# Kernel optimization log

Hardware: AMD Instinct MI355X
Metric: run time of the kernel (lower is better)

The kernel has to match this reference:

```python
import jax, jax.numpy as jnp
from jax import lax
import numpy as np

FEAT_STRIDE = 16
PRE_NMS_TOP_N = 2000
POST_NMS_TOP_N = 300
NMS_THRESH = 0.7


def _whctrs(a):
    w = a[2] - a[0] + 1.0
    h = a[3] - a[1] + 1.0
    return w, h, a[0] + 0.5 * (w - 1.0), a[1] + 0.5 * (h - 1.0)


def _mkanchors(ws, hs, x_ctr, y_ctr):
    ws = np.asarray(ws, dtype=np.float64)
    hs = np.asarray(hs, dtype=np.float64)
    return np.stack([x_ctr - 0.5 * (ws - 1.0), y_ctr - 0.5 * (hs - 1.0),
                     x_ctr + 0.5 * (ws - 1.0), y_ctr + 0.5 * (hs - 1.0)], axis=1)


def generate_anchors(base_size=16, ratios=np.array([0.5, 1.0, 2.0]), scales=np.array([8.0, 16.0, 32.0])):
    base = np.array([1.0, 1.0, float(base_size), float(base_size)]) - 1.0
    w, h, xc, yc = _whctrs(base)
    size = w * h
    ws = np.round(np.sqrt(size / ratios))
    hs = np.round(ws * ratios)
    ratio_anchors = _mkanchors(ws, hs, xc, yc)
    out = []
    for i in range(ratio_anchors.shape[0]):
        w_i, h_i, xc_i, yc_i = _whctrs(ratio_anchors[i])
        out.append(_mkanchors(w_i * scales, h_i * scales, xc_i, yc_i))
    return np.vstack(out).astype(np.float32)


ANCHORS = generate_anchors()  # [A=9, 4]
NUM_ANCHORS = ANCHORS.shape[0]


def _nms_keep(boxes, thresh):
    # boxes [N,4], already sorted by descending score; torchvision IoU convention.
    x1, y1, x2, y2 = boxes[:, 0], boxes[:, 1], boxes[:, 2], boxes[:, 3]
    areas = (x2 - x1) * (y2 - y1)
    xx1 = jnp.maximum(x1[:, None], x1[None, :])
    yy1 = jnp.maximum(y1[:, None], y1[None, :])
    xx2 = jnp.minimum(x2[:, None], x2[None, :])
    yy2 = jnp.minimum(y2[:, None], y2[None, :])
    inter = jnp.clip(xx2 - xx1, 0.0) * jnp.clip(yy2 - yy1, 0.0)
    iou = inter / (areas[:, None] + areas[None, :] - inter + 1e-9)
    n = boxes.shape[0]
    # sup[i, j] True => box i (higher score) suppresses later box j
    sup = (iou > thresh) & jnp.triu(jnp.ones((n, n), bool), 1)

    def body(i, keep):
        return keep & ~(keep[i] & sup[i])

    return lax.fori_loop(0, n, body, jnp.ones((n,), bool))


def setup_inputs() -> dict:
    key = jax.random.key(0)
    k1, k2 = jax.random.split(key)
    B, A, H, W = 8, NUM_ANCHORS, 128, 128
    scores = jax.random.normal(k1, (B, 2 * A, H, W), jnp.float32)
    bbox_deltas = jax.random.normal(k2, (B, 4 * A, H, W), jnp.float32) * 0.2
    im_h = float(H * FEAT_STRIDE)
    im_w = float(W * FEAT_STRIDE)
    im_info = jnp.tile(jnp.array([[im_h, im_w, 1.0]], jnp.float32), (B, 1))
    return {"scores": scores, "bbox_deltas": bbox_deltas, "im_info": im_info}


def reference(scores, bbox_deltas, im_info):
    B, _, H, W = scores.shape
    A = NUM_ANCHORS
    # --- anchor generation over the feature grid ---
    sx = jnp.arange(W, dtype=jnp.float32) * FEAT_STRIDE
    sy = jnp.arange(H, dtype=jnp.float32) * FEAT_STRIDE
    gx, gy = jnp.meshgrid(sx, sy)  # 'xy' indexing matches np.meshgrid default
    shifts = jnp.stack([gx.ravel(), gy.ravel(), gx.ravel(), gy.ravel()], axis=1)  # [K,4]
    anchors = (jnp.asarray(ANCHORS)[None, :, :] + shifts[:, None, :]).reshape(-1, 4)  # [K*A,4]

    obj_scores = scores[:, A:].transpose(0, 2, 3, 1).reshape(B, -1)   # [B, K*A]
    deltas = bbox_deltas.transpose(0, 2, 3, 1).reshape(B, -1, 4)      # [B, K*A, 4]

    # --- bbox_transform_inv ---
    widths = anchors[:, 2] - anchors[:, 0] + 1.0
    heights = anchors[:, 3] - anchors[:, 1] + 1.0
    ctr_x = anchors[:, 0] + 0.5 * widths
    ctr_y = anchors[:, 1] + 0.5 * heights
    dx, dy, dw, dh = deltas[..., 0], deltas[..., 1], deltas[..., 2], deltas[..., 3]
    pred_ctr_x = dx * widths + ctr_x
    pred_ctr_y = dy * heights + ctr_y
    pred_w = jnp.exp(dw) * widths
    pred_h = jnp.exp(dh) * heights
    proposals = jnp.stack([pred_ctr_x - 0.5 * pred_w, pred_ctr_y - 0.5 * pred_h,
                           pred_ctr_x + 0.5 * pred_w, pred_ctr_y + 0.5 * pred_h], axis=-1)

    # --- clip_boxes: im_info[b] = (h, w, scale) ---
    max_x = (im_info[:, 1] - 1.0)[:, None]
    max_y = (im_info[:, 0] - 1.0)[:, None]
    proposals = jnp.stack([
        jnp.clip(proposals[..., 0], 0.0, max_x),
        jnp.clip(proposals[..., 1], 0.0, max_y),
        jnp.clip(proposals[..., 2], 0.0, max_x),
        jnp.clip(proposals[..., 3], 0.0, max_y)], axis=-1)

    # --- pre-NMS top-k by score ---
    _, order = lax.top_k(obj_scores, PRE_NMS_TOP_N)                  # [B, pre]
    top_props = jnp.take_along_axis(proposals, order[..., None], axis=1)  # [B, pre, 4]

    # --- per-image greedy NMS (fixed-size, jit-compatible) ---
    keep = jax.vmap(lambda b: _nms_keep(b, NMS_THRESH))(top_props)   # [B, pre] bool
    sel = jnp.argsort(jnp.where(keep, 0, 1), axis=1, stable=True)[:, :POST_NMS_TOP_N]
    valid = jnp.take_along_axis(keep, sel, axis=1)                   # [B, post]
    out_boxes = jnp.take_along_axis(top_props, sel[..., None], axis=1) * valid[..., None].astype(top_props.dtype)

    batch_idx = jnp.broadcast_to(
        jnp.arange(B, dtype=out_boxes.dtype)[:, None, None], (B, POST_NMS_TOP_N, 1))
    return jnp.concatenate([batch_idx, out_boxes], axis=-1)  # [B, post_nms_topN, 5]
```

## Files before the change

kernel.cpp:

```cpp
#include <hip/hip_runtime.h>

#define NB 8
#define NA 9
#define NCELL (128 * 128)
#define NTOT (NCELL * NA)
#define PRE_K 2000
#define POST_K 300
#define PARTS 18
#define SLOT 512
#define THR_BIN 0x5FFu
#define NMS_TH 0.7f

__constant__ float c_aw[NA] = {184.f, 368.f, 736.f, 128.f, 256.f, 512.f, 88.f, 176.f, 352.f};
__constant__ float c_ah[NA] = {96.f, 192.f, 384.f, 128.f, 256.f, 512.f, 176.f, 352.f, 704.f};

__device__ __forceinline__ unsigned int sortable(float s) {
    unsigned int u = __float_as_uint(s);
    return (u & 0x80000000u) ? ~u : (u | 0x80000000u);
}

__device__ __forceinline__ unsigned long long shflx64(unsigned long long v, int m) {
    return __shfl_xor(v, m, 64);
}

__device__ __forceinline__ float4 decode_box(unsigned int i, const float* __restrict__ dbase,
                                             float maxx, float maxy) {
    unsigned int cell = i / 9u;
    unsigned int a = i - cell * 9u;
    int wx = (int)(cell & 127u), hy = (int)(cell >> 7);
    const float* dp = dbase + (size_t)(4u * a) * NCELL + (size_t)hy * 128 + wx;
    float dx = dp[0];
    float dy = dp[NCELL];
    float dw = dp[2 * NCELL];
    float dh = dp[3 * NCELL];
    float W_ = c_aw[a], H_ = c_ah[a];
    float cx = (float)(16 * wx + 8), cy = (float)(16 * hy + 8);
    float px = __fadd_rn(__fmul_rn(dx, W_), cx);
    float py = __fadd_rn(__fmul_rn(dy, H_), cy);
    float pw = __fmul_rn((float)exp((double)dw), W_);
    float ph = __fmul_rn((float)exp((double)dh), H_);
    float hw = __fmul_rn(0.5f, pw), hh = __fmul_rn(0.5f, ph);
    float x1 = __fsub_rn(px, hw), y1 = __fsub_rn(py, hh);
    float x2 = __fadd_rn(px, hw), y2 = __fadd_rn(py, hh);
    x1 = fminf(fmaxf(x1, 0.0f), maxx);
    y1 = fminf(fmaxf(y1, 0.0f), maxy);
    x2 = fminf(fmaxf(x2, 0.0f), maxx);
    y2 = fminf(fmaxf(y2, 0.0f), maxy);
    return make_float4(x1, y1, x2, y2);
}

__global__ __launch_bounds__(1024) void sweep_kernel(const float* __restrict__ scores,
                                                     unsigned int* __restrict__ h0out,
                                                     int* __restrict__ bcnt,
                                                     unsigned long long* __restrict__ buf) {
    __shared__ unsigned int h[2048];
    __shared__ unsigned long long lbuf[SLOT];
    __shared__ int lcnt;
    int b = blockIdx.y, part = blockIdx.x, tid = threadIdx.x;
    h[tid] = 0; h[tid + 1024] = 0;
    if (tid == 0) lcnt = 0;
    __syncthreads();
    const float4* sp4 = (const float4*)(scores + (size_t)b * 18 * NCELL + (size_t)NA * NCELL);
    int base4 = part * 2048;
#pragma unroll
    for (int e = 0; e < 2; ++e) {
        int t4 = base4 + e * 1024 + tid;
        float4 v = sp4[t4];
        float el[4] = {v.x, v.y, v.z, v.w};
#pragma unroll
        for (int j = 0; j < 4; ++j) {
            unsigned int u = sortable(el[j]);
            atomicAdd(&h[u >> 21], 1u);
            if ((u >> 21) >= THR_BIN) {
                int idx4 = t4 * 4 + j;
                int a = idx4 >> 14;
                int cell = idx4 & 16383;
                unsigned int i = (unsigned int)cell * 9u + (unsigned int)a;
                int pos = atomicAdd(&lcnt, 1);
                if (pos < SLOT)
                    lbuf[pos] = ((unsigned long long)u << 32) |
                                (unsigned long long)(0xFFFFFFFFu - i);
            }
        }
    }
    __syncthreads();
    unsigned int* o = h0out + ((size_t)(b * PARTS + part)) * 2048;
    o[tid] = h[tid];
    o[tid + 1024] = h[tid + 1024];
    if (tid == 0) bcnt[b * PARTS + part] = lcnt;
    int m = min(lcnt, SLOT);
    for (int t = tid; t < m; t += 1024)
        buf[((size_t)(b * PARTS + part)) * SLOT + t] = lbuf[t];
}

#define SHFL_STEP(J)                                                          \
    {                                                                         \
        int d_ = (J) >> 1;                                                    \
        bool keepMax = (((tid & d_) == 0) == (((2u * (unsigned)tid) & k) == 0)); \
        unsigned long long pa = shflx64(va, d_);                              \
        unsigned long long pb = shflx64(vb, d_);                              \
        va = keepMax ? (va > pa ? va : pa) : (va < pa ? va : pa);             \
        vb = keepMax ? (vb > pb ? vb : pb) : (vb < pb ? vb : pb);             \
    }
#define LOCAL_STEP()                                                          \
    {                                                                         \
        bool desc = (((2u * (unsigned)tid) & k) == 0);                        \
        unsigned long long lo = va < vb ? va : vb;                            \
        unsigned long long hi = va < vb ? vb : va;                            \
        va = desc ? hi : lo; vb = desc ? lo : hi;                             \
    }

__global__ __launch_bounds__(1024) void sortdec_kernel(const float* __restrict__ scores,
                                                       const unsigned int* __restrict__ h0out,
                                                       const int* __restrict__ bcnt,
                                                       const unsigned long long* __restrict__ buf,
                                                       unsigned int* __restrict__ topidx) {
    __shared__ unsigned long long s[4096];
    __shared__ unsigned int wpart[16], wexcl[16];
    __shared__ unsigned int h128[128];
    __shared__ int sbc[PARTS];
    __shared__ unsigned int sh_piv, sh_spiv;
    __shared__ unsigned int sh_need;
    __shared__ int sh_ok, fcnt;
    int b = blockIdx.x, tid = threadIdx.x;
    int lane = tid & 63, wid = tid >> 6;
    unsigned int* thr = (unsigned int*)s;

    if (tid < PARTS) sbc[tid] = bcnt[b * PARTS + tid];
    if (tid == 0) { sh_ok = 1; fcnt = 0; }

    unsigned int c0 = 0, c1 = 0;
#pragma unroll
    for (int p = 0; p < PARTS; ++p) {
        const unsigned int* hp = h0out + ((size_t)(b * PARTS + p)) * 2048;
        uint2 v = *(const uint2*)&hp[2 * tid];
        c0 += v.x; c1 += v.y;
    }
    unsigned int sum = c0 + c1;
#pragma unroll
    for (int off = 1; off < 64; off <<= 1) {
        unsigned int v = __shfl_down(sum, off, 64);
        if (lane + off < 64) sum += v;
    }
    if (lane == 0) wpart[wid] = sum;
    __syncthreads();
    if (tid < 16) {
        unsigned int e = 0;
        for (int w = tid + 1; w < 16; ++w) e += wpart[w];
        wexcl[tid] = e;
    }
    __syncthreads();
    unsigned int self = sum + wexcl[wid];
    thr[tid] = self;
    __syncthreads();
    unsigned int above = (tid < 1023) ? thr[tid + 1] : 0u;
    if (self >= (unsigned)PRE_K && above < (unsigned)PRE_K) {
        if (above + c1 >= (unsigned)PRE_K) {
            sh_piv = (unsigned)(2 * tid + 1); sh_need = (unsigned)(PRE_K)-above;
        } else {
            sh_piv = (unsigned)(2 * tid); sh_need = (unsigned)(PRE_K)-above - c1;
        }
    }
    __syncthreads();
    unsigned int piv = sh_piv;
    if (tid < PARTS && sbc[tid] > SLOT) sh_ok = 0;
    if (tid == 0 && piv < THR_BIN) sh_ok = 0;
    if (tid < 128) h128[tid] = 0;
    __syncthreads();
    int ok = sh_ok;

    if (ok) {
        for (int t = tid; t < PARTS * SLOT; t += 1024) {
            int p = t >> 9, off = t & (SLOT - 1);
            if (off < sbc[p]) {
                unsigned long long e = buf[((size_t)(b * PARTS + p)) * SLOT + off];
                unsigned int u = (unsigned int)(e >> 32);
                if ((u >> 21) == piv) atomicAdd(&h128[(u >> 14) & 127u], 1u);
            }
        }
    } else {
        const float4* sp4 = (const float4*)(scores + (size_t)b * 18 * NCELL + (size_t)NA * NCELL);
        for (int t = tid; t < NTOT / 4; t += 1024) {
            float4 v = sp4[t];
            unsigned int u;
            u = sortable(v.x); if ((u >> 21) == piv) atomicAdd(&h128[(u >> 14) & 127u], 1u);
            u = sortable(v.y); if ((u >> 21) == piv) atomicAdd(&h128[(u >> 14) & 127u], 1u);
            u = sortable(v.z); if ((u >> 21) == piv) atomicAdd(&h128[(u >> 14) & 127u], 1u);
            u = sortable(v.w); if ((u >> 21) == piv) atomicAdd(&h128[(u >> 14) & 127u], 1u);
        }
    }
    __syncthreads();
    if (tid < 64) {
        unsigned int d0 = h128[2 * lane], d1 = h128[2 * lane + 1];
        unsigned int rs = d0 + d1;
#pragma unroll
        for (int off = 1; off < 64; off <<= 1) {
            unsigned int v = __shfl_down(rs, off, 64);
            if (lane + off < 64) rs += v;
        }
        unsigned int rab = __shfl_down(rs, 1, 64);
        if (lane == 63) rab = 0;
        unsigned int need0 = sh_need;
        if (rs >= need0 && rab < need0) {
            unsigned int d = (rab + d1 >= need0) ? (unsigned)(2 * lane + 1) : (unsigned)(2 * lane);
            sh_spiv = ((piv << 7) | d) << 14;
        }
    }
    __syncthreads();
    unsigned int spiv = sh_spiv;

    if (ok) {
        for (int t = tid; t < PARTS * SLOT; t += 1024) {
            int p = t >> 9, off = t & (SLOT - 1);
            if (off < sbc[p]) {
                unsigned long long e = buf[((size_t)(b * PARTS + p)) * SLOT + off];
                if ((unsigned int)(e >> 32) >= spiv) {
                    int pos = atomicAdd(&fcnt, 1);
                    if (pos < 4096) s[pos] = e;
                }
            }
        }
    } else {
        const float4* sp4 = (const float4*)(scores + (size_t)b * 18 * NCELL + (size_t)NA * NCELL);
        for (int t4 = tid; t4 < NTOT / 4; t4 += 1024) {
            float4 v = sp4[t4];
            float el[4] = {v.x, v.y, v.z, v.w};
#pragma unroll
            for (int j = 0; j < 4; ++j) {
                unsigned int u = sortable(el[j]);
                if (u >= spiv) {
                    int idx4 = t4 * 4 + j;
                    int a = idx4 >> 14;
                    int cell = idx4 & 16383;
                    unsigned int i = (unsigned int)cell * 9u + (unsigned int)a;
                    int pos = atomicAdd(&fcnt, 1);
                    if (pos < 4096)
                        s[pos] = ((unsigned long long)u << 32) |
                                 (unsigned long long)(0xFFFFFFFFu - i);
                }
            }
        }
    }
    __syncthreads();
    int n2 = min(fcnt, 4096);
    int SZ = (n2 <= 2048) ? 2048 : 4096;
    for (int t = tid; t < SZ; t += 1024)
        if (t >= n2) s[t] = 0ULL;
    __syncthreads();

    if (SZ == 2048) {
        unsigned long long va = s[2 * tid], vb = s[2 * tid + 1];
#pragma unroll
        for (unsigned k = 2; k <= 128; k <<= 1) {
#pragma unroll
            for (unsigned j = k >> 1; j >= 2; j >>= 1) SHFL_STEP(j)
            LOCAL_STEP()
        }
        for (unsigned k = 256; k <= 2048; k <<= 1) {
            s[2 * tid] = va; s[2 * tid + 1] = vb;
            __syncthreads();
            for (unsigned j = k >> 1; j >= 128; j >>= 1) {
                for (int t = tid; t < 2048; t += 1024) {
                    int ixj = t ^ (int)j;
                    if (ixj > t) {
                        unsigned long long x = s[t], y = s[ixj];
                        if ((((unsigned)t & k) == 0) ? (x < y) : (x > y)) { s[t] = y; s[ixj] = x; }
                    }
                }
                __syncthreads();
            }
            va = s[2 * tid]; vb = s[2 * tid + 1];
#pragma unroll
            for (unsigned j = 64; j >= 2; j >>= 1) SHFL_STEP(j)
            LOCAL_STEP()
        }
        s[2 * tid] = va; s[2 * tid + 1] = vb;
        __syncthreads();
    } else {
        for (int k = 2; k <= 4096; k <<= 1) {
            for (int j = k >> 1; j > 0; j >>= 1) {
                for (int t = tid; t < 4096; t += 1024) {
                    int ixj = t ^ j;
                    if (ixj > t) {
                        unsigned long long x = s[t], y = s[ixj];
                        if (((t & k) == 0) ? (x < y) : (x > y)) { s[t] = y; s[ixj] = x; }
                    }
                }
                __syncthreads();
            }
        }
    }
    for (int r = tid; r < PRE_K; r += 1024)
        topidx[(size_t)b * PRE_K + r] = 0xFFFFFFFFu - (unsigned int)(s[r] & 0xFFFFFFFFu);
}

__global__ void mask_kernel(const unsigned int* __restrict__ topidx,
                            const float* __restrict__ deltas,
                            const float* __restrict__ im_info,
                            unsigned long long* __restrict__ colm) {
    int iT = blockIdx.x, jT = blockIdx.y, b = blockIdx.z;
    if (iT > jT) return;
    __shared__ float4 ib[64];
    int t = threadIdx.x;
    float maxx = __fsub_rn(im_info[b * 3 + 1], 1.0f);
    float maxy = __fsub_rn(im_info[b * 3 + 0], 1.0f);
    const float* dbase = deltas + (size_t)b * 36 * NCELL;
    const unsigned int* ti = topidx + (size_t)b * PRE_K;
    int i0 = iT * 64;
    ib[t] = (i0 + t < PRE_K) ? decode_box(ti[i0 + t], dbase, maxx, maxy)
                             : make_float4(0.f, 0.f, -1.f, -1.f);
    int j = jT * 64 + t;
    bool jv = j < PRE_K;
    float4 jb = jv ? decode_box(ti[j], dbase, maxx, maxy) : make_float4(0.f, 0.f, -1.f, -1.f);
    __syncthreads();
    if (!jv) return;
    float barea = __fmul_rn(__fsub_rn(jb.z, jb.x), __fsub_rn(jb.w, jb.y));
    unsigned long long m = 0ULL;
    for (int ii = 0; ii < 64; ++ii) {
        int i = i0 + ii;
        if (i < j) {
            float4 c = ib[ii];
            float aarea = __fmul_rn(__fsub_rn(c.z, c.x), __fsub_rn(c.w, c.y));
            float xx1 = fmaxf(c.x, jb.x), yy1 = fmaxf(c.y, jb.y);
            float xx2 = fminf(c.z, jb.z), yy2 = fminf(c.w, jb.w);
            float iw = fmaxf(__fsub_rn(xx2, xx1), 0.0f);
            float ih = fmaxf(__fsub_rn(yy2, yy1), 0.0f);
            float inter = __fmul_rn(iw, ih);
            float denom = __fadd_rn(__fsub_rn(__fadd_rn(aarea, barea), inter), 1e-9f);
            float iou = __fdiv_rn(inter, denom);
            if (iou > NMS_TH) m |= (1ULL << ii);
        }
    }
    colm[((size_t)b * 32 + iT) * 2048 + j] = m;
}

#define PROCESS_TILE(K, BUF)                                                   \
    {                                                                          \
        unsigned long long diag = 0ULL;                                        \
        _Pragma("unroll") for (int q = 0; q < 32; ++q)                         \
            if (q == (K)) diag = BUF[q];                                       \
        int j = (K) * 64 + lane;                                               \
        bool alive_me = (((dead >> (K)) & 1u) == 0u) && (j < PRE_K);           \
        unsigned long long alive = __ballot(alive_me);                         \
        unsigned long long keptw = 0ULL;                                       \
        while (alive) {                                                        \
            int i = __builtin_ctzll(alive);                                    \
            keptw |= (1ULL << i);                                              \
            if (lane == 0 && total < POST_K) keeplist[total] = (K) * 64 + i;   \
            total++;                                                           \
            if (total >= POST_K) { done = true; break; }                       \
            unsigned long long sup = __ballot(((diag >> i) & 1ULL) != 0ULL);   \
            alive &= ~sup;                                                     \
            alive &= ~keptw;                                                   \
        }                                                                      \
        _Pragma("unroll") for (int q = 0; q < 32; ++q)                         \
            if (q > (K) && ((BUF[q] & keptw) != 0ULL)) dead |= (1u << q);      \
    }

__global__ __launch_bounds__(64) void scan_kernel(const unsigned long long* __restrict__ colm,
                                                  const unsigned int* __restrict__ topidx,
                                                  const float* __restrict__ deltas,
                                                  const float* __restrict__ im_info,
                                                  float* __restrict__ out) {
    __shared__ int keeplist[POST_K];
    int b = blockIdx.x, lane = threadIdx.x;
    const unsigned long long* cb = colm + (size_t)b * 32 * 2048;
    unsigned int dead = 0;
    int total = 0;
    bool done = false;
    unsigned long long bufA[32], bufB[32];
#pragma unroll
    for (int q = 0; q < 32; ++q) bufA[q] = cb[q * 64 + lane];
    for (int kk = 0; kk < 16 && !done; ++kk) {
        int k0 = 2 * kk;
#pragma unroll
        for (int q = 0; q < 32; ++q)
            bufB[q] = cb[(size_t)(k0 + 1) * 2048 + q * 64 + lane];
        PROCESS_TILE(k0, bufA)
        if (done) break;
        int k1 = k0 + 1;
        if (k1 + 1 < 32) {
#pragma unroll
            for (int q = 0; q < 32; ++q)
                bufA[q] = cb[(size_t)(k1 + 1) * 2048 + q * 64 + lane];
        }
        PROCESS_TILE(k1, bufB)
    }
    __syncthreads();
    int K = min(total, POST_K);
    float maxx = __fsub_rn(im_info[b * 3 + 1], 1.0f);
    float maxy = __fsub_rn(im_info[b * 3 + 0], 1.0f);
    const float* dbase = deltas + (size_t)b * 36 * NCELL;
    const unsigned int* ti = topidx + (size_t)b * PRE_K;
    for (int r = lane; r < POST_K; r += 64) {
        float4 v = make_float4(0.f, 0.f, 0.f, 0.f);
        if (r < K) v = decode_box(ti[keeplist[r]], dbase, maxx, maxy);
        float* o = out + ((size_t)b * POST_K + r) * 5;
        o[0] = (float)b;
        o[1] = v.x;
        o[2] = v.y;
        o[3] = v.z;
        o[4] = v.w;
    }
}

extern "C" void kernel_launch(void* const* d_in, const int* in_sizes, int n_in,
                              void* d_out, int out_size, void* d_ws, size_t ws_size,
                              hipStream_t stream) {
    const float* scores = (const float*)d_in[0];
    const float* deltas = (const float*)d_in[1];
    const float* im_info = (const float*)d_in[2];
    float* out = (float*)d_out;
    char* ws = (char*)d_ws;

    unsigned int* h0out = (unsigned int*)(ws + 0);
    int* bcnt = (int*)(ws + 1179648);
    unsigned long long* buf = (unsigned long long*)(ws + 1180672);
    unsigned int* topidx = (unsigned int*)(ws + 1770496);
    unsigned long long* colm = (unsigned long long*)(ws + 1834496);

    hipLaunchKernelGGL(sweep_kernel, dim3(PARTS, NB), dim3(1024), 0, stream,
                       scores, h0out, bcnt, buf);
    hipLaunchKernelGGL(sortdec_kernel, dim3(NB), dim3(1024), 0, stream,
                       scores, h0out, bcnt, buf, topidx);
    hipLaunchKernelGGL(mask_kernel, dim3(32, 32, NB), dim3(64), 0, stream,
                       topidx, deltas, im_info, colm);
    hipLaunchKernelGGL(scan_kernel, dim3(NB), dim3(64), 0, stream,
                       colm, topidx, deltas, im_info, out);
}
```

Measured before the change: 106.9 us.

## Drop full-histogram output from sweep and precompute decoded boxes in separate kernel

The sweep kernel no longer builds or writes a 2048-bin histogram per partition. The sort kernel instead builds its coarse histogram from only the candidate buffer, falling back to a full rescan when the buffer overflows or holds fewer than PRE_K entries. A new decode kernel decodes the 2000 top boxes per image once into a float4 array, which the mask and scan kernels then read instead of recomputing exp-based decoding per tile. This adds one kernel launch and removes redundant double-precision exp work and histogram atomics and traffic.

```diff
diff --git a/kernel.cpp b/kernel.cpp
--- a/kernel.cpp
+++ b/kernel.cpp
@@ -23,12 +23,276 @@
     return __shfl_xor(v, m, 64);
 }
 
-__device__ __forceinline__ float4 decode_box(unsigned int i, const float* __restrict__ dbase,
-                                             float maxx, float maxy) {
+__global__ __launch_bounds__(1024) void sweep_kernel(const float* __restrict__ scores,
+                                                     int* __restrict__ bcnt,
+                                                     unsigned long long* __restrict__ buf) {
+    __shared__ unsigned long long lbuf[SLOT];
+    __shared__ int lcnt;
+    int b = blockIdx.y, part = blockIdx.x, tid = threadIdx.x;
+    if (tid == 0) lcnt = 0;
+    __syncthreads();
+    const float4* sp4 = (const float4*)(scores + (size_t)b * 18 * NCELL + (size_t)NA * NCELL);
+    int base4 = part * 2048;
+#pragma unroll
+    for (int e = 0; e < 2; ++e) {
+        int t4 = base4 + e * 1024 + tid;
+        float4 v = sp4[t4];
+        float el[4] = {v.x, v.y, v.z, v.w};
+#pragma unroll
+        for (int j = 0; j < 4; ++j) {
+            unsigned int u = sortable(el[j]);
+            if ((u >> 21) >= THR_BIN) {
+                int idx4 = t4 * 4 + j;
+                int a = idx4 >> 14;
+                int cell = idx4 & 16383;
+                unsigned int i = (unsigned int)cell * 9u + (unsigned int)a;
+                int pos = atomicAdd(&lcnt, 1);
+                if (pos < SLOT)
+                    lbuf[pos] = ((unsigned long long)u << 32) |
+                                (unsigned long long)(0xFFFFFFFFu - i);
+            }
+        }
+    }
+    __syncthreads();
+    if (tid == 0) bcnt[b * PARTS + part] = lcnt;
+    int m = min(lcnt, SLOT);
+    for (int t = tid; t < m; t += 1024)
+        buf[((size_t)(b * PARTS + part)) * SLOT + t] = lbuf[t];
+}
+
+#define SHFL_STEP(J)                                                          \
+    {                                                                         \
+        int d_ = (J) >> 1;                                                    \
+        bool keepMax = (((tid & d_) == 0) == (((2u * (unsigned)tid) & k) == 0)); \
+        unsigned long long pa = shflx64(va, d_);                              \
+        unsigned long long pb = shflx64(vb, d_);                              \
+        va = keepMax ? (va > pa ? va : pa) : (va < pa ? va : pa);             \
+        vb = keepMax ? (vb > pb ? vb : pb) : (vb < pb ? vb : pb);             \
+    }
+#define LOCAL_STEP()                                                          \
+    {                                                                         \
+        bool desc = (((2u * (unsigned)tid) & k) == 0);                        \
+        unsigned long long lo = va < vb ? va : vb;                            \
+        unsigned long long hi = va < vb ? vb : va;                            \
+        va = desc ? hi : lo; vb = desc ? lo : hi;                             \
+    }
+
+__global__ __launch_bounds__(1024) void sortdec_kernel(const float* __restrict__ scores,
+                                                       const int* __restrict__ bcnt,
+                                                       const unsigned long long* __restrict__ buf,
+                                                       unsigned int* __restrict__ topidx) {
+    __shared__ unsigned long long s[4096];
+    __shared__ unsigned int wpart[16], wexcl[16];
+    __shared__ unsigned int h128[128];
+    __shared__ int sbc[PARTS];
+    __shared__ unsigned int sh_piv, sh_spiv;
+    __shared__ unsigned int sh_need;
+    __shared__ int sh_ok, fcnt;
+    int b = blockIdx.x, tid = threadIdx.x;
+    int lane = tid & 63, wid = tid >> 6;
+    unsigned int* hist2 = (unsigned int*)s;
+    unsigned int* thr = ((unsigned int*)s) + 2048;
+
+    if (tid < PARTS) sbc[tid] = bcnt[b * PARTS + tid];
+    if (tid == 0) fcnt = 0;
+    hist2[tid] = 0; hist2[tid + 1024] = 0;
+    __syncthreads();
+    if (tid == 0) {
+        int okv = 1, tot = 0;
+        for (int p = 0; p < PARTS; ++p) { if (sbc[p] > SLOT) okv = 0; tot += sbc[p]; }
+        if (tot < PRE_K) okv = 0;
+        sh_ok = okv;
+    }
+    __syncthreads();
+    int ok = sh_ok;
+
+    if (ok) {
+        for (int t = tid; t < PARTS * SLOT; t += 1024) {
+            int p = t >> 9, off = t & (SLOT - 1);
+            if (off < sbc[p]) {
+                unsigned int u = (unsigned int)(buf[((size_t)(b * PARTS + p)) * SLOT + off] >> 32);
+                atomicAdd(&hist2[u >> 21], 1u);
+            }
+        }
+    } else {
+        const float4* sp4 = (const float4*)(scores + (size_t)b * 18 * NCELL + (size_t)NA * NCELL);
+        for (int t = tid; t < NTOT / 4; t += 1024) {
+            float4 v = sp4[t];
+            atomicAdd(&hist2[sortable(v.x) >> 21], 1u);
+            atomicAdd(&hist2[sortable(v.y) >> 21], 1u);
+            atomicAdd(&hist2[sortable(v.z) >> 21], 1u);
+            atomicAdd(&hist2[sortable(v.w) >> 21], 1u);
+        }
+    }
+    __syncthreads();
+    unsigned int c0 = hist2[2 * tid], c1 = hist2[2 * tid + 1];
+    unsigned int sum = c0 + c1;
+#pragma unroll
+    for (int off = 1; off < 64; off <<= 1) {
+        unsigned int v = __shfl_down(sum, off, 64);
+        if (lane + off < 64) sum += v;
+    }
+    if (lane == 0) wpart[wid] = sum;
+    __syncthreads();
+    if (tid < 16) {
+        unsigned int e = 0;
+        for (int w = tid + 1; w < 16; ++w) e += wpart[w];
+        wexcl[tid] = e;
+    }
+    __syncthreads();
+    unsigned int self = sum + wexcl[wid];
+    thr[tid] = self;
+    __syncthreads();
+    unsigned int above = (tid < 1023) ? thr[tid + 1] : 0u;
+    if (self >= (unsigned)PRE_K && above < (unsigned)PRE_K) {
+        if (above + c1 >= (unsigned)PRE_K) {
+            sh_piv = (unsigned)(2 * tid + 1); sh_need = (unsigned)(PRE_K)-above;
+        } else {
+            sh_piv = (unsigned)(2 * tid); sh_need = (unsigned)(PRE_K)-above - c1;
+        }
+    }
+    if (tid < 128) h128[tid] = 0;
+    __syncthreads();
+    unsigned int piv = sh_piv;
+
+    if (ok) {
+        for (int t = tid; t < PARTS * SLOT; t += 1024) {
+            int p = t >> 9, off = t & (SLOT - 1);
+            if (off < sbc[p]) {
+                unsigned long long e = buf[((size_t)(b * PARTS + p)) * SLOT + off];
+                unsigned int u = (unsigned int)(e >> 32);
+                if ((u >> 21) == piv) atomicAdd(&h128[(u >> 14) & 127u], 1u);
+            }
+        }
+    } else {
+        const float4* sp4 = (const float4*)(scores + (size_t)b * 18 * NCELL + (size_t)NA * NCELL);
+        for (int t = tid; t < NTOT / 4; t += 1024) {
+            float4 v = sp4[t];
+            unsigned int u;
+            u = sortable(v.x); if ((u >> 21) == piv) atomicAdd(&h128[(u >> 14) & 127u], 1u);
+            u = sortable(v.y); if ((u >> 21) == piv) atomicAdd(&h128[(u >> 14) & 127u], 1u);
+            u = sortable(v.z); if ((u >> 21) == piv) atomicAdd(&h128[(u >> 14) & 127u], 1u);
+            u = sortable(v.w); if ((u >> 21) == piv) atomicAdd(&h128[(u >> 14) & 127u], 1u);
+        }
+    }
+    __syncthreads();
+    if (tid < 64) {
+        unsigned int d0 = h128[2 * lane], d1 = h128[2 * lane + 1];
+        unsigned int rs = d0 + d1;
+#pragma unroll
+        for (int off = 1; off < 64; off <<= 1) {
+            unsigned int v = __shfl_down(rs, off, 64);
+            if (lane + off < 64) rs += v;
+        }
+        unsigned int rab = __shfl_down(rs, 1, 64);
+        if (lane == 63) rab = 0;
+        unsigned int need0 = sh_need;
+        if (rs >= need0 && rab < need0) {
+            unsigned int d = (rab + d1 >= need0) ? (unsigned)(2 * lane + 1) : (unsigned)(2 * lane);
+            sh_spiv = ((piv << 7) | d) << 14;
+        }
+    }
+    __syncthreads();
+    unsigned int spiv = sh_spiv;
+
+    if (ok) {
+        for (int t = tid; t < PARTS * SLOT; t += 1024) {
+            int p = t >> 9, off = t & (SLOT - 1);
+            if (off < sbc[p]) {
+                unsigned long long e = buf[((size_t)(b * PARTS + p)) * SLOT + off];
+                if ((unsigned int)(e >> 32) >= spiv) {
+                    int pos = atomicAdd(&fcnt, 1);
+                    if (pos < 4096) s[pos] = e;
+                }
+            }
+        }
+    } else {
+        const float4* sp4 = (const float4*)(scores + (size_t)b * 18 * NCELL + (size_t)NA * NCELL);
+        for (int t4 = tid; t4 < NTOT / 4; t4 += 1024) {
+            float4 v = sp4[t4];
+            float el[4] = {v.x, v.y, v.z, v.w};
+#pragma unroll
+            for (int j = 0; j < 4; ++j) {
+                unsigned int u = sortable(el[j]);
+                if (u >= spiv) {
+                    int idx4 = t4 * 4 + j;
+                    int a = idx4 >> 14;
+                    int cell = idx4 & 16383;
+                    unsigned int i = (unsigned int)cell * 9u + (unsigned int)a;
+                    int pos = atomicAdd(&fcnt, 1);
+                    if (pos < 4096)
+                        s[pos] = ((unsigned long long)u << 32) |
+                                 (unsigned long long)(0xFFFFFFFFu - i);
+                }
+            }
+        }
+    }
+    __syncthreads();
+    int n2 = min(fcnt, 4096);
+    int SZ = (n2 <= 2048) ? 2048 : 4096;
+    for (int t = tid; t < SZ; t += 1024)
+        if (t >= n2) s[t] = 0ULL;
+    __syncthreads();
+
+    if (SZ == 2048) {
+        unsigned long long va = s[2 * tid], vb = s[2 * tid + 1];
+#pragma unroll
+        for (unsigned k = 2; k <= 128; k <<= 1) {
+#pragma unroll
+            for (unsigned j = k >> 1; j >= 2; j >>= 1) SHFL_STEP(j)
+            LOCAL_STEP()
+        }
+        for (unsigned k = 256; k <= 2048; k <<= 1) {
+            s[2 * tid] = va; s[2 * tid + 1] = vb;
+            __syncthreads();
+            for (unsigned j = k >> 1; j >= 128; j >>= 1) {
+                for (int t = tid; t < 2048; t += 1024) {
+                    int ixj = t ^ (int)j;
+                    if (ixj > t) {
+                        unsigned long long x = s[t], y = s[ixj];
+                        if ((((unsigned)t & k) == 0) ? (x < y) : (x > y)) { s[t] = y; s[ixj] = x; }
+                    }
+                }
+                __syncthreads();
+            }
+            va = s[2 * tid]; vb = s[2 * tid + 1];
+#pragma unroll
+            for (unsigned j = 64; j >= 2; j >>= 1) SHFL_STEP(j)
+            LOCAL_STEP()
+        }
+        s[2 * tid] = va; s[2 * tid + 1] = vb;
+        __syncthreads();
+    } else {
+        for (int k = 2; k <= 4096; k <<= 1) {
+            for (int j = k >> 1; j > 0; j >>= 1) {
+                for (int t = tid; t < 4096; t += 1024) {
+                    int ixj = t ^ j;
+                    if (ixj > t) {
+                        unsigned long long x = s[t], y = s[ixj];
+                        if (((t & k) == 0) ? (x < y) : (x > y)) { s[t] = y; s[ixj] = x; }
+                    }
+                }
+                __syncthreads();
+            }
+        }
+    }
+    for (int r = tid; r < PRE_K; r += 1024)
+        topidx[(size_t)b * PRE_K + r] = 0xFFFFFFFFu - (unsigned int)(s[r] & 0xFFFFFFFFu);
+}
+
+__global__ void decode_kernel(const unsigned int* __restrict__ topidx,
+                              const float* __restrict__ deltas,
+                              const float* __restrict__ im_info,
+                              float4* __restrict__ props) {
+    int gid = blockIdx.x * 256 + threadIdx.x;
+    if (gid >= NB * PRE_K) return;
+    int b = gid / PRE_K;
+    unsigned int i = topidx[gid];
     unsigned int cell = i / 9u;
     unsigned int a = i - cell * 9u;
     int wx = (int)(cell & 127u), hy = (int)(cell >> 7);
-    const float* dp = dbase + (size_t)(4u * a) * NCELL + (size_t)hy * 128 + wx;
+    const float* dp = deltas + (size_t)b * 36 * NCELL + (size_t)(4u * a) * NCELL +
+                      (size_t)hy * 128 + wx;
     float dx = dp[0];
     float dy = dp[NCELL];
     float dw = dp[2 * NCELL];
@@ -42,278 +306,27 @@
     float hw = __fmul_rn(0.5f, pw), hh = __fmul_rn(0.5f, ph);
     float x1 = __fsub_rn(px, hw), y1 = __fsub_rn(py, hh);
     float x2 = __fadd_rn(px, hw), y2 = __fadd_rn(py, hh);
+    float maxx = __fsub_rn(im_info[b * 3 + 1], 1.0f);
+    float maxy = __fsub_rn(im_info[b * 3 + 0], 1.0f);
     x1 = fminf(fmaxf(x1, 0.0f), maxx);
     y1 = fminf(fmaxf(y1, 0.0f), maxy);
     x2 = fminf(fmaxf(x2, 0.0f), maxx);
     y2 = fminf(fmaxf(y2, 0.0f), maxy);
-    return make_float4(x1, y1, x2, y2);
-}
-
-__global__ __launch_bounds__(1024) void sweep_kernel(const float* __restrict__ scores,
-                                                     unsigned int* __restrict__ h0out,
-                                                     int* __restrict__ bcnt,
-                                                     unsigned long long* __restrict__ buf) {
-    __shared__ unsigned int h[2048];
-    __shared__ unsigned long long lbuf[SLOT];
-    __shared__ int lcnt;
-    int b = blockIdx.y, part = blockIdx.x, tid = threadIdx.x;
-    h[tid] = 0; h[tid + 1024] = 0;
-    if (tid == 0) lcnt = 0;
-    __syncthreads();
-    const float4* sp4 = (const float4*)(scores + (size_t)b * 18 * NCELL + (size_t)NA * NCELL);
-    int base4 = part * 2048;
-#pragma unroll
-    for (int e = 0; e < 2; ++e) {
-        int t4 = base4 + e * 1024 + tid;
-        float4 v = sp4[t4];
-        float el[4] = {v.x, v.y, v.z, v.w};
-#pragma unroll
-        for (int j = 0; j < 4; ++j) {
-            unsigned int u = sortable(el[j]);
-            atomicAdd(&h[u >> 21], 1u);
-            if ((u >> 21) >= THR_BIN) {
-                int idx4 = t4 * 4 + j;
-                int a = idx4 >> 14;
-                int cell = idx4 & 16383;
-                unsigned int i = (unsigned int)cell * 9u + (unsigned int)a;
-                int pos = atomicAdd(&lcnt, 1);
-                if (pos < SLOT)
-                    lbuf[pos] = ((unsigned long long)u << 32) |
-                                (unsigned long long)(0xFFFFFFFFu - i);
-            }
-        }
-    }
-    __syncthreads();
-    unsigned int* o = h0out + ((size_t)(b * PARTS + part)) * 2048;
-    o[tid] = h[tid];
-    o[tid + 1024] = h[tid + 1024];
-    if (tid == 0) bcnt[b * PARTS + part] = lcnt;
-    int m = min(lcnt, SLOT);
-    for (int t = tid; t < m; t += 1024)
-        buf[((size_t)(b * PARTS + part)) * SLOT + t] = lbuf[t];
-}
-
-#define SHFL_STEP(J)                                                          \
-    {                                                                         \
-        int d_ = (J) >> 1;                                                    \
-        bool keepMax = (((tid & d_) == 0) == (((2u * (unsigned)tid) & k) == 0)); \
-        unsigned long long pa = shflx64(va, d_);                              \
-        unsigned long long pb = shflx64(vb, d_);                              \
-        va = keepMax ? (va > pa ? va : pa) : (va < pa ? va : pa);             \
-        vb = keepMax ? (vb > pb ? vb : pb) : (vb < pb ? vb : pb);             \
-    }
-#define LOCAL_STEP()                                                          \
-    {                                                                         \
-        bool desc = (((2u * (unsigned)tid) & k) == 0);                        \
-        unsigned long long lo = va < vb ? va : vb;                            \
-        unsigned long long hi = va < vb ? vb : va;                            \
-        va = desc ? hi : lo; vb = desc ? lo : hi;                             \
-    }
-
-__global__ __launch_bounds__(1024) void sortdec_kernel(const float* __restrict__ scores,
-                                                       const unsigned int* __restrict__ h0out,
-                                                       const int* __restrict__ bcnt,
-                                                       const unsigned long long* __restrict__ buf,
-                                                       unsigned int* __restrict__ topidx) {
-    __shared__ unsigned long long s[4096];
-    __shared__ unsigned int wpart[16], wexcl[16];
-    __shared__ unsigned int h128[128];
-    __shared__ int sbc[PARTS];
-    __shared__ unsigned int sh_piv, sh_spiv;
-    __shared__ unsigned int sh_need;
-    __shared__ int sh_ok, fcnt;
-    int b = blockIdx.x, tid = threadIdx.x;
-    int lane = tid & 63, wid = tid >> 6;
-    unsigned int* thr = (unsigned int*)s;
-
-    if (tid < PARTS) sbc[tid] = bcnt[b * PARTS + tid];
-    if (tid == 0) { sh_ok = 1; fcnt = 0; }
-
-    unsigned int c0 = 0, c1 = 0;
-#pragma unroll
-    for (int p = 0; p < PARTS; ++p) {
-        const unsigned int* hp = h0out + ((size_t)(b * PARTS + p)) * 2048;
-        uint2 v = *(const uint2*)&hp[2 * tid];
-        c0 += v.x; c1 += v.y;
-    }
-    unsigned int sum = c0 + c1;
-#pragma unroll
-    for (int off = 1; off < 64; off <<= 1) {
-        unsigned int v = __shfl_down(sum, off, 64);
-        if (lane + off < 64) sum += v;
-    }
-    if (lane == 0) wpart[wid] = sum;
-    __syncthreads();
-    if (tid < 16) {
-        unsigned int e = 0;
-        for (int w = tid + 1; w < 16; ++w) e += wpart[w];
-        wexcl[tid] = e;
-    }
-    __syncthreads();
-    unsigned int self = sum + wexcl[wid];
-    thr[tid] = self;
-    __syncthreads();
-    unsigned int above = (tid < 1023) ? thr[tid + 1] : 0u;
-    if (self >= (unsigned)PRE_K && above < (unsigned)PRE_K) {
-        if (above + c1 >= (unsigned)PRE_K) {
-            sh_piv = (unsigned)(2 * tid + 1); sh_need = (unsigned)(PRE_K)-above;
-        } else {
-            sh_piv = (unsigned)(2 * tid); sh_need = (unsigned)(PRE_K)-above - c1;
-        }
-    }
-    __syncthreads();
-    unsigned int piv = sh_piv;
-    if (tid < PARTS && sbc[tid] > SLOT) sh_ok = 0;
-    if (tid == 0 && piv < THR_BIN) sh_ok = 0;
-    if (tid < 128) h128[tid] = 0;
-    __syncthreads();
-    int ok = sh_ok;
-
-    if (ok) {
-        for (int t = tid; t < PARTS * SLOT; t += 1024) {
-            int p = t >> 9, off = t & (SLOT - 1);
-            if (off < sbc[p]) {
-                unsigned long long e = buf[((size_t)(b * PARTS + p)) * SLOT + off];
-                unsigned int u = (unsigned int)(e >> 32);
-                if ((u >> 21) == piv) atomicAdd(&h128[(u >> 14) & 127u], 1u);
-            }
-        }
-    } else {
-        const float4* sp4 = (const float4*)(scores + (size_t)b * 18 * NCELL + (size_t)NA * NCELL);
-        for (int t = tid; t < NTOT / 4; t += 1024) {
-            float4 v = sp4[t];
-            unsigned int u;
-            u = sortable(v.x); if ((u >> 21) == piv) atomicAdd(&h128[(u >> 14) & 127u], 1u);
-            u = sortable(v.y); if ((u >> 21) == piv) atomicAdd(&h128[(u >> 14) & 127u], 1u);
-            u = sortable(v.z); if ((u >> 21) == piv) atomicAdd(&h128[(u >> 14) & 127u], 1u);
-            u = sortable(v.w); if ((u >> 21) == piv) atomicAdd(&h128[(u >> 14) & 127u], 1u);
-        }
-    }
-    __syncthreads();
-    if (tid < 64) {
-        unsigned int d0 = h128[2 * lane], d1 = h128[2 * lane + 1];
-        unsigned int rs = d0 + d1;
-#pragma unroll
-        for (int off = 1; off < 64; off <<= 1) {
-            unsigned int v = __shfl_down(rs, off, 64);
-            if (lane + off < 64) rs += v;
-        }
-        unsigned int rab = __shfl_down(rs, 1, 64);
-        if (lane == 63) rab = 0;
-        unsigned int need0 = sh_need;
-        if (rs >= need0 && rab < need0) {
-            unsigned int d = (rab + d1 >= need0) ? (unsigned)(2 * lane + 1) : (unsigned)(2 * lane);
-            sh_spiv = ((piv << 7) | d) << 14;
-        }
-    }
-    __syncthreads();
-    unsigned int spiv = sh_spiv;
-
-    if (ok) {
-        for (int t = tid; t < PARTS * SLOT; t += 1024) {
-            int p = t >> 9, off = t & (SLOT - 1);
-            if (off < sbc[p]) {
-                unsigned long long e = buf[((size_t)(b * PARTS + p)) * SLOT + off];
-                if ((unsigned int)(e >> 32) >= spiv) {
-                    int pos = atomicAdd(&fcnt, 1);
-                    if (pos < 4096) s[pos] = e;
-                }
-            }
-        }
-    } else {
-        const float4* sp4 = (const float4*)(scores + (size_t)b * 18 * NCELL + (size_t)NA * NCELL);
-        for (int t4 = tid; t4 < NTOT / 4; t4 += 1024) {
-            float4 v = sp4[t4];
-            float el[4] = {v.x, v.y, v.z, v.w};
-#pragma unroll
-            for (int j = 0; j < 4; ++j) {
-                unsigned int u = sortable(el[j]);
-                if (u >= spiv) {
-                    int idx4 = t4 * 4 + j;
-                    int a = idx4 >> 14;
-                    int cell = idx4 & 16383;
-                    unsigned int i = (unsigned int)cell * 9u + (unsigned int)a;
-                    int pos = atomicAdd(&fcnt, 1);
-                    if (pos < 4096)
-                        s[pos] = ((unsigned long long)u << 32) |
-                                 (unsigned long long)(0xFFFFFFFFu - i);
-                }
-            }
-        }
-    }
-    __syncthreads();
-    int n2 = min(fcnt, 4096);
-    int SZ = (n2 <= 2048) ? 2048 : 4096;
-    for (int t = tid; t < SZ; t += 1024)
-        if (t >= n2) s[t] = 0ULL;
-    __syncthreads();
-
-    if (SZ == 2048) {
-        unsigned long long va = s[2 * tid], vb = s[2 * tid + 1];
-#pragma unroll
-        for (unsigned k = 2; k <= 128; k <<= 1) {
-#pragma unroll
-            for (unsigned j = k >> 1; j >= 2; j >>= 1) SHFL_STEP(j)
-            LOCAL_STEP()
-        }
-        for (unsigned k = 256; k <= 2048; k <<= 1) {
-            s[2 * tid] = va; s[2 * tid + 1] = vb;
-            __syncthreads();
-            for (unsigned j = k >> 1; j >= 128; j >>= 1) {
-                for (int t = tid; t < 2048; t += 1024) {
-                    int ixj = t ^ (int)j;
-                    if (ixj > t) {
-                        unsigned long long x = s[t], y = s[ixj];
-                        if ((((unsigned)t & k) == 0) ? (x < y) : (x > y)) { s[t] = y; s[ixj] = x; }
-                    }
-                }
-                __syncthreads();
-            }
-            va = s[2 * tid]; vb = s[2 * tid + 1];
-#pragma unroll
-            for (unsigned j = 64; j >= 2; j >>= 1) SHFL_STEP(j)
-            LOCAL_STEP()
-        }
-        s[2 * tid] = va; s[2 * tid + 1] = vb;
-        __syncthreads();
-    } else {
-        for (int k = 2; k <= 4096; k <<= 1) {
-            for (int j = k >> 1; j > 0; j >>= 1) {
-                for (int t = tid; t < 4096; t += 1024) {
-                    int ixj = t ^ j;
-                    if (ixj > t) {
-                        unsigned long long x = s[t], y = s[ixj];
-                        if (((t & k) == 0) ? (x < y) : (x > y)) { s[t] = y; s[ixj] = x; }
-                    }
-                }
-                __syncthreads();
-            }
-        }
-    }
-    for (int r = tid; r < PRE_K; r += 1024)
-        topidx[(size_t)b * PRE_K + r] = 0xFFFFFFFFu - (unsigned int)(s[r] & 0xFFFFFFFFu);
-}
-
-__global__ void mask_kernel(const unsigned int* __restrict__ topidx,
-                            const float* __restrict__ deltas,
-                            const float* __restrict__ im_info,
+    props[gid] = make_float4(x1, y1, x2, y2);
+}
+
+__global__ void mask_kernel(const float4* __restrict__ boxes,
                             unsigned long long* __restrict__ colm) {
     int iT = blockIdx.x, jT = blockIdx.y, b = blockIdx.z;
     if (iT > jT) return;
     __shared__ float4 ib[64];
     int t = threadIdx.x;
-    float maxx = __fsub_rn(im_info[b * 3 + 1], 1.0f);
-    float maxy = __fsub_rn(im_info[b * 3 + 0], 1.0f);
-    const float* dbase = deltas + (size_t)b * 36 * NCELL;
-    const unsigned int* ti = topidx + (size_t)b * PRE_K;
     int i0 = iT * 64;
-    ib[t] = (i0 + t < PRE_K) ? decode_box(ti[i0 + t], dbase, maxx, maxy)
-                             : make_float4(0.f, 0.f, -1.f, -1.f);
+    ib[t] = (i0 + t < PRE_K) ? boxes[(size_t)b * PRE_K + i0 + t] : make_float4(0.f, 0.f, -1.f, -1.f);
+    __syncthreads();
     int j = jT * 64 + t;
-    bool jv = j < PRE_K;
-    float4 jb = jv ? decode_box(ti[j], dbase, maxx, maxy) : make_float4(0.f, 0.f, -1.f, -1.f);
-    __syncthreads();
-    if (!jv) return;
+    if (j >= PRE_K) return;
+    float4 jb = boxes[(size_t)b * PRE_K + j];
     float barea = __fmul_rn(__fsub_rn(jb.z, jb.x), __fsub_rn(jb.w, jb.y));
     unsigned long long m = 0ULL;
     for (int ii = 0; ii < 64; ++ii) {
@@ -358,9 +371,7 @@
     }
 
 __global__ __launch_bounds__(64) void scan_kernel(const unsigned long long* __restrict__ colm,
-                                                  const unsigned int* __restrict__ topidx,
-                                                  const float* __restrict__ deltas,
-                                                  const float* __restrict__ im_info,
+                                                  const float4* __restrict__ boxes,
                                                   float* __restrict__ out) {
     __shared__ int keeplist[POST_K];
     int b = blockIdx.x, lane = threadIdx.x;
@@ -386,15 +397,11 @@
         }
         PROCESS_TILE(k1, bufB)
     }
-    __syncthreads();
     int K = min(total, POST_K);
-    float maxx = __fsub_rn(im_info[b * 3 + 1], 1.0f);
-    float maxy = __fsub_rn(im_info[b * 3 + 0], 1.0f);
-    const float* dbase = deltas + (size_t)b * 36 * NCELL;
-    const unsigned int* ti = topidx + (size_t)b * PRE_K;
+    const float4* bb = boxes + (size_t)b * PRE_K;
     for (int r = lane; r < POST_K; r += 64) {
         float4 v = make_float4(0.f, 0.f, 0.f, 0.f);
-        if (r < K) v = decode_box(ti[keeplist[r]], dbase, maxx, maxy);
+        if (r < K) v = bb[keeplist[r]];
         float* o = out + ((size_t)b * POST_K + r) * 5;
         o[0] = (float)b;
         o[1] = v.x;
@@ -413,18 +420,18 @@
     float* out = (float*)d_out;
     char* ws = (char*)d_ws;
 
-    unsigned int* h0out = (unsigned int*)(ws + 0);
-    int* bcnt = (int*)(ws + 1179648);
-    unsigned long long* buf = (unsigned long long*)(ws + 1180672);
-    unsigned int* topidx = (unsigned int*)(ws + 1770496);
-    unsigned long long* colm = (unsigned long long*)(ws + 1834496);
+    int* bcnt = (int*)(ws + 0);
+    unsigned long long* buf = (unsigned long long*)(ws + 1024);
+    unsigned int* topidx = (unsigned int*)(ws + 590848);
+    float4* props = (float4*)(ws + 654848);
+    unsigned long long* colm = (unsigned long long*)(ws + 910848);
 
     hipLaunchKernelGGL(sweep_kernel, dim3(PARTS, NB), dim3(1024), 0, stream,
-                       scores, h0out, bcnt, buf);
+                       scores, bcnt, buf);
     hipLaunchKernelGGL(sortdec_kernel, dim3(NB), dim3(1024), 0, stream,
-                       scores, h0out, bcnt, buf, topidx);
-    hipLaunchKernelGGL(mask_kernel, dim3(32, 32, NB), dim3(64), 0, stream,
-                       topidx, deltas, im_info, colm);
-    hipLaunchKernelGGL(scan_kernel, dim3(NB), dim3(64), 0, stream,
-                       colm, topidx, deltas, im_info, out);
-}
+                       scores, bcnt, buf, topidx);
+    hipLaunchKernelGGL(decode_kernel, dim3((NB * PRE_K + 255) / 256), dim3(256), 0, stream,
+                       topidx, deltas, im_info, props);
+    hipLaunchKernelGGL(mask_kernel, dim3(32, 32, NB), dim3(64), 0, stream, props, colm);
+    hipLaunchKernelGGL(scan_kernel, dim3(NB), dim3(64), 0, stream, colm, props, out);
+}
```

Measured after the change: 100.1 us. 1.07x faster.
